# Performance work log

Measured on AMD Instinct MI355X. Metric: run time of the kernel, lower is better.

## Reference

```python
import jax, jax.numpy as jnp
import numpy as np

E, N, F = 50000, 25000, 32

def setup_inputs() -> dict:
    key = jax.random.key(0)
    ks = jax.random.split(key, 8)
    efeat = jax.random.normal(ks[0], (E, F), dtype=jnp.float32) * 0.2
    initial_efeats = jax.random.normal(ks[1], (E, F), dtype=jnp.float32) * 0.2
    # msg_fn / attn_fn: Linear(F, F*F)
    Wm = jax.random.normal(ks[2], (F * F, F), dtype=jnp.float32) * 0.05
    bm = jnp.zeros((F * F,), dtype=jnp.float32)
    Wa = jax.random.normal(ks[3], (F * F, F), dtype=jnp.float32) * 0.05
    ba = jnp.zeros((F * F,), dtype=jnp.float32)
    src = jax.random.randint(ks[4], (E,), 0, N, dtype=jnp.int32)
    dst = jax.random.randint(ks[5], (E,), 0, N, dtype=jnp.int32)
    return {"efeat": efeat, "initial_efeats": initial_efeats, "Wm": Wm, "bm": bm,
            "Wa": Wa, "ba": ba, "src": src, "dst": dst, "num_nodes": N}

def reference(efeat, initial_efeats, Wm, bm, Wa, ba, src, dst, num_nodes):
    e, f = efeat.shape
    # edge-conditioned transform matrices: [E, F, F]
    w_m = (efeat @ Wm.T + bm).reshape(e, f, f)
    w_a = (efeat @ Wa.T + ba).reshape(e, f, f)
    h = efeat[:, :, None]                 # [E, F, 1]
    ih = initial_efeats[:, :, None]       # [E, F, 1]
    e1 = w_m * h                          # [E, F, F]
    exp_e2 = jnp.exp(w_a * h)             # [E, F, F]
    initial_e1 = w_m * ih
    exp_initial_e2 = jnp.exp(w_a * ih)
    # scatter-sum exp weights to destination nodes, gather back at src
    sum_exp_node = jax.ops.segment_sum(exp_e2, dst, num_segments=num_nodes)  # [N, F, F]
    sum_exp = sum_exp_node[src] - exp_e2 + exp_initial_e2
    h1 = exp_e2 * e1
    initial_h1 = exp_initial_e2 * initial_e1
    m_node = jax.ops.segment_sum(h1, dst, num_segments=num_nodes)            # [N, F, F]
    h2 = (m_node[src] - h1 + initial_h1) / sum_exp
    return h2.sum(axis=1)                 # [E, F]
```

## Files before the change

kernel.cpp:

```cpp
#include <hip/hip_runtime.h>
#include <hip/hip_fp16.h>
#include <math.h>
#include <stdint.h>


#define FDIM   32
#define NNODES 25000

typedef __attribute__((ext_vector_type(8))) short bf16x8;
typedef __attribute__((ext_vector_type(4))) float f32x4;

__device__ __forceinline__ unsigned short f2bf(float f) {
    unsigned u = __float_as_uint(f);
    return (unsigned short)((u + 0x7FFFu + ((u >> 16) & 1u)) >> 16);
}
__device__ __forceinline__ float hlo(unsigned v) {
    return __half2float(__ushort_as_half((unsigned short)v));
}
__device__ __forceinline__ unsigned pk2(float m, float a) {
    unsigned um = (unsigned)__half_as_ushort(__float2half(m));
    unsigned ua = (unsigned)__half_as_ushort(__float2half(a));
    return (um >> 8) | (ua & 0xFF00u);
}

__global__ __launch_bounds__(256) void zero_f4(float4* __restrict__ p, int n4) {
    int i = blockIdx.x * blockDim.x + threadIdx.x;
    int stride = gridDim.x * blockDim.x;
    float4 z = make_float4(0.f, 0.f, 0.f, 0.f);
    for (; i < n4; i += stride) p[i] = z;
}

__global__ __launch_bounds__(256) void k_hist(
    const int* __restrict__ src, const int* __restrict__ dst,
    int* __restrict__ cnt_src, int* __restrict__ cnt_dst, int E) {
    int e = blockIdx.x * blockDim.x + threadIdx.x;
    if (e < E) {
        atomicAdd(&cnt_dst[dst[e]], 1);
        atomicAdd(&cnt_src[src[e]], 1);
    }
}

__global__ __launch_bounds__(256) void k_scan2(
    const int* __restrict__ cnt_dst, int* __restrict__ off_dst, int* __restrict__ cur_dst,
    const int* __restrict__ cnt_src, int* __restrict__ off_src, int* __restrict__ cur_src,
    int n) {
    const int* cnt = blockIdx.x ? cnt_src : cnt_dst;
    int* off = blockIdx.x ? off_src : off_dst;
    int* cur = blockIdx.x ? cur_src : cur_dst;
    __shared__ int wsum[4];
    __shared__ int carry_sh;
    const int tid = threadIdx.x, lane = tid & 63, w = tid >> 6;
    if (tid == 0) carry_sh = 0;
    __syncthreads();
    for (int base = 0; base < n; base += 4096) {
        int i0 = base + tid * 16;
        int v[16];
        int s = 0;
#pragma unroll
        for (int k = 0; k < 16; ++k) {
            v[k] = (i0 + k < n) ? cnt[i0 + k] : 0;
            s += v[k];
        }
        int inc = s;
        for (int d = 1; d < 64; d <<= 1) {
            int t = __shfl_up(inc, d, 64);
            if (lane >= d) inc += t;
        }
        if (lane == 63) wsum[w] = inc;
        __syncthreads();
        int wbase = 0;
        for (int k = 0; k < w; ++k) wbase += wsum[k];
        int carry = carry_sh;
        int excl = carry + wbase + inc - s;
#pragma unroll
        for (int k = 0; k < 16; ++k) {
            if (i0 + k < n) { off[i0 + k] = excl; cur[i0 + k] = excl; }
            excl += v[k];
        }
        __syncthreads();
        if (tid == 255) carry_sh = carry + wbase + inc;
    }
    __syncthreads();
    if (tid == 0) off[n] = carry_sh;
}

__global__ __launch_bounds__(256) void k_scatter(
    const int* __restrict__ src, const int* __restrict__ dst,
    int* __restrict__ cur_src, int* __restrict__ cur_dst,
    int* __restrict__ eb_src, int* __restrict__ eb_dst, int E) {
    int e = blockIdx.x * blockDim.x + threadIdx.x;
    if (e < E) {
        int p = atomicAdd(&cur_dst[dst[e]], 1); eb_dst[p] = e;
        int q = atomicAdd(&cur_src[src[e]], 1); eb_src[q] = e;
    }
}

__global__ __launch_bounds__(256) void prep_w(
    const float* __restrict__ Wm, const float* __restrict__ Wa,
    short* __restrict__ wbuf) {
    int idx = blockIdx.x * blockDim.x + threadIdx.x;
    if (idx >= 2 * 64 * 64) return;
    int mat  = idx >> 12;
    int jt   = (idx >> 6) & 63;
    int lane = idx & 63;
    const float* W = mat ? Wa : Wm;
    const float* s = W + (size_t)(jt * 16 + (lane & 15)) * FDIM + (lane >> 4) * 8;
    bf16x8 v;
#pragma unroll
    for (int t = 0; t < 8; ++t) v[t] = (short)f2bf(s[t]);
    *(bf16x8*)(wbuf + (size_t)idx * 8) = v;
}

__global__ __launch_bounds__(256) void gemm(
    const float* __restrict__ efeat,
    const float* __restrict__ bm, const float* __restrict__ ba,
    const short* __restrict__ wbuf,
    unsigned* __restrict__ buf, int E)
{
    const int lane = threadIdx.x & 63;
    const int wid  = threadIdx.x >> 6;
    const int et   = blockIdx.x * 4 + wid;
    if (et * 16 >= E) return;
    const int r16 = lane & 15;
    const int kq  = lane >> 4;

    const float* xa = efeat + (size_t)(et * 16 + r16) * FDIM + kq * 8;
    bf16x8 xfrag;
#pragma unroll
    for (int t = 0; t < 8; ++t) xfrag[t] = (short)f2bf(xa[t]);

    const int e = et * 16 + r16;
    unsigned* bout = buf + ((size_t)e << 9);

    for (int m = 0; m < 16; ++m) {
        unsigned P[4][4];
#pragma unroll
        for (int p = 0; p < 4; ++p) {
            const int jt = m * 4 + p;
            bf16x8 wfm = *(const bf16x8*)(wbuf + ((size_t)(jt)      * 64 + lane) * 8);
            bf16x8 wfa = *(const bf16x8*)(wbuf + ((size_t)(64 + jt) * 64 + lane) * 8);
            const int jb = jt * 16 + kq * 4;
            const float4 bm4 = *(const float4*)(bm + jb);
            const float4 ba4 = *(const float4*)(ba + jb);
            f32x4 accm = {bm4.x, bm4.y, bm4.z, bm4.w};
            f32x4 acca = {ba4.x, ba4.y, ba4.z, ba4.w};
            accm = __builtin_amdgcn_mfma_f32_16x16x32_bf16(wfm, xfrag, accm, 0, 0, 0);
            acca = __builtin_amdgcn_mfma_f32_16x16x32_bf16(wfa, xfrag, acca, 0, 0, 0);
#pragma unroll
            for (int r = 0; r < 4; ++r) P[p][r] = pk2(accm[r], acca[r]);
        }
        uint4 sa, sb;
        sa.x = P[0][0] | (P[2][0] << 16);
        sa.y = P[0][1] | (P[2][1] << 16);
        sa.z = P[0][2] | (P[2][2] << 16);
        sa.w = P[0][3] | (P[2][3] << 16);
        sb.x = P[1][0] | (P[3][0] << 16);
        sb.y = P[1][1] | (P[3][1] << 16);
        sb.z = P[1][2] | (P[3][2] << 16);
        sb.w = P[1][3] | (P[3][3] << 16);
        *(uint4*)(bout + m * 32 + kq * 4)      = sa;
        *(uint4*)(bout + m * 32 + 16 + kq * 4) = sb;
    }
}

__global__ __launch_bounds__(256) void consume(
    const float* __restrict__ efeat, const float* __restrict__ ifeat,
    const unsigned* __restrict__ buf,
    const int* __restrict__ off_dst, const int* __restrict__ eb_dst,
    const int* __restrict__ off_src, const int* __restrict__ eb_src,
    float* __restrict__ out)
{
    const int tid = threadIdx.x;
    const int l   = tid & 63;
    const int wid = tid >> 6;
    const int n   = blockIdx.x * 4 + wid;
    if (n >= NNODES) return;

    const int a0 = off_dst[n], a1 = off_dst[n + 1];
    const int b0 = off_src[n], b1 = off_src[n + 1];
    const int din = a1 - a0, dout = b1 - b0;
    if (dout == 0) return;

    int eid = (l < 32) ? eb_dst[a0 + l] : eb_src[b0 + (l - 32)];
    const int half = l & 1;
    const int j2   = l >> 1;
    const int mb   = half * 8;

    float S[16], M[16];
#pragma unroll
    for (int t = 0; t < 16; ++t) { S[t] = 0.f; M[t] = 0.f; }

    for (int t = 0; t < din; ++t) {
        int e = (t < 32) ? __shfl(eid, t, 64) : eb_dst[a0 + t];
        e = __builtin_amdgcn_readfirstlane(e);
        const unsigned* bp = buf + ((size_t)e << 9) + j2;
        const float* xr = efeat + ((size_t)e << 5) + half * 16;
        float xf[16];
        {
            float4 q0 = *(const float4*)(xr + 0);
            float4 q1 = *(const float4*)(xr + 4);
            float4 q2 = *(const float4*)(xr + 8);
            float4 q3 = *(const float4*)(xr + 12);
            xf[0]=q0.x; xf[1]=q0.y; xf[2]=q0.z; xf[3]=q0.w;
            xf[4]=q1.x; xf[5]=q1.y; xf[6]=q1.z; xf[7]=q1.w;
            xf[8]=q2.x; xf[9]=q2.y; xf[10]=q2.z; xf[11]=q2.w;
            xf[12]=q3.x; xf[13]=q3.y; xf[14]=q3.z; xf[15]=q3.w;
        }
#pragma unroll
        for (int s = 0; s < 8; ++s) {
            unsigned d = bp[(mb + s) * 32];
            float am0 = hlo(d << 8),  aa0 = hlo(d);
            float am1 = hlo(d >> 8),  aa1 = hlo(d >> 16);
            float xi0 = xf[2 * s], xi1 = xf[2 * s + 1];
            float ea = __expf(aa0 * xi0);
            float eb = __expf(aa1 * xi1);
            S[2 * s]     += ea;  M[2 * s]     = fmaf(ea, am0 * xi0, M[2 * s]);
            S[2 * s + 1] += eb;  M[2 * s + 1] = fmaf(eb, am1 * xi1, M[2 * s + 1]);
        }
    }

    for (int t = 0; t < dout; ++t) {
        int e = (t < 32) ? __shfl(eid, 32 + t, 64) : eb_src[b0 + t];
        e = __builtin_amdgcn_readfirstlane(e);
        const unsigned* bp = buf + ((size_t)e << 9) + j2;
        const float* xr  = efeat + ((size_t)e << 5) + half * 16;
        const float* x0r = ifeat + ((size_t)e << 5) + half * 16;
        float xf[16], x0f[16];
        {
            float4 q0 = *(const float4*)(xr + 0);
            float4 q1 = *(const float4*)(xr + 4);
            float4 q2 = *(const float4*)(xr + 8);
            float4 q3 = *(const float4*)(xr + 12);
            xf[0]=q0.x; xf[1]=q0.y; xf[2]=q0.z; xf[3]=q0.w;
            xf[4]=q1.x; xf[5]=q1.y; xf[6]=q1.z; xf[7]=q1.w;
            xf[8]=q2.x; xf[9]=q2.y; xf[10]=q2.z; xf[11]=q2.w;
            xf[12]=q3.x; xf[13]=q3.y; xf[14]=q3.z; xf[15]=q3.w;
            float4 p0 = *(const float4*)(x0r + 0);
            float4 p1 = *(const float4*)(x0r + 4);
            float4 p2 = *(const float4*)(x0r + 8);
            float4 p3 = *(const float4*)(x0r + 12);
            x0f[0]=p0.x; x0f[1]=p0.y; x0f[2]=p0.z; x0f[3]=p0.w;
            x0f[4]=p1.x; x0f[5]=p1.y; x0f[6]=p1.z; x0f[7]=p1.w;
            x0f[8]=p2.x; x0f[9]=p2.y; x0f[10]=p2.z; x0f[11]=p2.w;
            x0f[12]=p3.x; x0f[13]=p3.y; x0f[14]=p3.z; x0f[15]=p3.w;
        }
        float osum = 0.f;
#pragma unroll
        for (int s = 0; s < 8; ++s) {
            unsigned d = bp[(mb + s) * 32];
            float am0 = hlo(d << 8),  aa0 = hlo(d);
            float am1 = hlo(d >> 8),  aa1 = hlo(d >> 16);
#define PROC(T, AM, AA)                                                 \
            {                                                           \
                float xi   = xf[T];                                     \
                float x0i  = x0f[T];                                    \
                float e2   = __expf((AA) * xi);                         \
                float h1   = e2 * ((AM) * xi);                          \
                float ei2  = __expf((AA) * x0i);                        \
                float ih1  = ei2 * ((AM) * x0i);                        \
                float den  = (S[T] - e2) + ei2;                         \
                float num  = (M[T] - h1) + ih1;                         \
                float h2   = num * __builtin_amdgcn_rcpf(den);          \
                osum += isfinite(h2) ? h2 : 0.f;                        \
            }
            PROC(2 * s,     am0, aa0);
            PROC(2 * s + 1, am1, aa1);
#undef PROC
        }
        osum += __shfl_xor(osum, 1, 64);
        if (half == 0) out[((size_t)e << 5) + j2] = osum;
    }
}

extern "C" void kernel_launch(void* const* d_in, const int* in_sizes, int n_in,
                              void* d_out, int out_size, void* d_ws, size_t ws_size,
                              hipStream_t stream) {
    const float* efeat = (const float*)d_in[0];
    const float* ifeat = (const float*)d_in[1];
    const float* Wm    = (const float*)d_in[2];
    const float* bm    = (const float*)d_in[3];
    const float* Wa    = (const float*)d_in[4];
    const float* ba    = (const float*)d_in[5];
    const int*   src   = (const int*)d_in[6];
    const int*   dst   = (const int*)d_in[7];
    const int E = in_sizes[6];
    const int N = NNODES;
    float* out = (float*)d_out;

    int* cnt_dst = (int*)d_ws;
    int* cnt_src = cnt_dst + N;
    int* off_dst = cnt_src + N;
    int* off_src = off_dst + (N + 1);
    int* cur_dst = off_src + (N + 1);
    int* cur_src = cur_dst + N;
    int* eb_dst  = cur_src + N;
    int* eb_src  = eb_dst + E;
    short* wbuf  = (short*)(((uintptr_t)(eb_src + E) + 255) & ~(uintptr_t)255);
    unsigned* buf =
        (unsigned*)(((uintptr_t)(wbuf + 2 * 64 * 64 * 8) + 255) & ~(uintptr_t)255);

    zero_f4<<<64, 256, 0, stream>>>((float4*)cnt_dst, (2 * N) / 4);
    k_hist<<<(E + 255) / 256, 256, 0, stream>>>(src, dst, cnt_src, cnt_dst, E);
    k_scan2<<<2, 256, 0, stream>>>(cnt_dst, off_dst, cur_dst,
                                   cnt_src, off_src, cur_src, N);
    k_scatter<<<(E + 255) / 256, 256, 0, stream>>>(src, dst, cur_src, cur_dst,
                                                   eb_src, eb_dst, E);
    prep_w<<<32, 256, 0, stream>>>(Wm, Wa, wbuf);

    const int etiles = (E + 15) / 16;
    gemm<<<(etiles + 3) / 4, 256, 0, stream>>>(efeat, bm, ba, wbuf, buf, E);
    consume<<<(NNODES + 3) / 4, 256, 0, stream>>>(efeat, ifeat, buf,
                                                  off_dst, eb_dst,
                                                  off_src, eb_src, out);
}
```

Measured before the change: 244.2 us.

## Prescale GEMM outputs by edge features and software-pipeline consume loads

The GEMM epilogue now stores w_a*x*log2(e) and w_m*x in place of the raw weights, plus a per-edge fp16 ratio x0/x. This lets consume drop its efeat/ifeat loads and use exp2 directly. The consume loops are double-buffered so the next edge's packed data is loaded while the current one is processed. The risk is precision loss from storing prescaled values in the 8-bit packed format and from the ratio, which becomes huge or infinite when x is near zero.

```diff
diff --git a/kernel.cpp b/kernel.cpp
--- a/kernel.cpp
+++ b/kernel.cpp
@@ -17,11 +17,16 @@
 __device__ __forceinline__ float hlo(unsigned v) {
     return __half2float(__ushort_as_half((unsigned short)v));
 }
-__device__ __forceinline__ unsigned pk2(float m, float a) {
-    unsigned um = (unsigned)__half_as_ushort(__float2half(m));
-    unsigned ua = (unsigned)__half_as_ushort(__float2half(a));
-    return (um >> 8) | (ua & 0xFF00u);
-}
+__device__ __forceinline__ unsigned pk2(float q, float p) {
+    unsigned uq = (unsigned)__half_as_ushort(__float2half(q));
+    unsigned up = (unsigned)__half_as_ushort(__float2half(p));
+    return (uq >> 8) | (up & 0xFF00u);
+}
+#if __has_builtin(__builtin_amdgcn_exp2f)
+__device__ __forceinline__ float ex2(float x) { return __builtin_amdgcn_exp2f(x); }
+#else
+__device__ __forceinline__ float ex2(float x) { return exp2f(x); }
+#endif
 
 __global__ __launch_bounds__(256) void zero_f4(float4* __restrict__ p, int n4) {
     int i = blockIdx.x * blockDim.x + threadIdx.x;
@@ -112,10 +117,10 @@
 }
 
 __global__ __launch_bounds__(256) void gemm(
-    const float* __restrict__ efeat,
+    const float* __restrict__ efeat, const float* __restrict__ ifeat,
     const float* __restrict__ bm, const float* __restrict__ ba,
     const short* __restrict__ wbuf,
-    unsigned* __restrict__ buf, int E)
+    unsigned* __restrict__ buf, unsigned* __restrict__ ratio, int E)
 {
     const int lane = threadIdx.x & 63;
     const int wid  = threadIdx.x >> 6;
@@ -123,16 +128,20 @@
     if (et * 16 >= E) return;
     const int r16 = lane & 15;
     const int kq  = lane >> 4;
-
-    const float* xa = efeat + (size_t)(et * 16 + r16) * FDIM + kq * 8;
+    const int e   = et * 16 + r16;
+
+    const float* xrow  = efeat + ((size_t)e << 5);
+    const float* x0row = ifeat + ((size_t)e << 5);
+
+    const float* xa = xrow + kq * 8;
     bf16x8 xfrag;
 #pragma unroll
     for (int t = 0; t < 8; ++t) xfrag[t] = (short)f2bf(xa[t]);
 
-    const int e = et * 16 + r16;
     unsigned* bout = buf + ((size_t)e << 9);
 
     for (int m = 0; m < 16; ++m) {
+        float2 xe = *(const float2*)(xrow + 2 * m);
         unsigned P[4][4];
 #pragma unroll
         for (int p = 0; p < 4; ++p) {
@@ -146,8 +155,11 @@
             f32x4 acca = {ba4.x, ba4.y, ba4.z, ba4.w};
             accm = __builtin_amdgcn_mfma_f32_16x16x32_bf16(wfm, xfrag, accm, 0, 0, 0);
             acca = __builtin_amdgcn_mfma_f32_16x16x32_bf16(wfa, xfrag, acca, 0, 0, 0);
-#pragma unroll
-            for (int r = 0; r < 4; ++r) P[p][r] = pk2(accm[r], acca[r]);
+            const float xi  = (p >> 1) ? xe.y : xe.x;
+            const float xil = xi * 1.44269504f;
+#pragma unroll
+            for (int r = 0; r < 4; ++r)
+                P[p][r] = pk2(acca[r] * xil, accm[r] * xi);
         }
         uint4 sa, sb;
         sa.x = P[0][0] | (P[2][0] << 16);
@@ -160,12 +172,20 @@
         sb.w = P[1][3] | (P[3][3] << 16);
         *(uint4*)(bout + m * 32 + kq * 4)      = sa;
         *(uint4*)(bout + m * 32 + 16 + kq * 4) = sb;
+
+        if (kq == 0) {
+            float2 x0e = *(const float2*)(x0row + 2 * m);
+            float r0 = x0e.x * __builtin_amdgcn_rcpf(xe.x);
+            float r1 = x0e.y * __builtin_amdgcn_rcpf(xe.y);
+            unsigned h0 = (unsigned)__half_as_ushort(__float2half(r0));
+            unsigned h1 = (unsigned)__half_as_ushort(__float2half(r1));
+            ratio[((size_t)e << 4) + m] = h0 | (h1 << 16);
+        }
     }
 }
 
 __global__ __launch_bounds__(256) void consume(
-    const float* __restrict__ efeat, const float* __restrict__ ifeat,
-    const unsigned* __restrict__ buf,
+    const unsigned* __restrict__ buf, const unsigned* __restrict__ ratio,
     const int* __restrict__ off_dst, const int* __restrict__ eb_dst,
     const int* __restrict__ off_src, const int* __restrict__ eb_src,
     float* __restrict__ out)
@@ -190,86 +210,76 @@
 #pragma unroll
     for (int t = 0; t < 16; ++t) { S[t] = 0.f; M[t] = 0.f; }
 
-    for (int t = 0; t < din; ++t) {
-        int e = (t < 32) ? __shfl(eid, t, 64) : eb_dst[a0 + t];
-        e = __builtin_amdgcn_readfirstlane(e);
-        const unsigned* bp = buf + ((size_t)e << 9) + j2;
-        const float* xr = efeat + ((size_t)e << 5) + half * 16;
-        float xf[16];
-        {
-            float4 q0 = *(const float4*)(xr + 0);
-            float4 q1 = *(const float4*)(xr + 4);
-            float4 q2 = *(const float4*)(xr + 8);
-            float4 q3 = *(const float4*)(xr + 12);
-            xf[0]=q0.x; xf[1]=q0.y; xf[2]=q0.z; xf[3]=q0.w;
-            xf[4]=q1.x; xf[5]=q1.y; xf[6]=q1.z; xf[7]=q1.w;
-            xf[8]=q2.x; xf[9]=q2.y; xf[10]=q2.z; xf[11]=q2.w;
-            xf[12]=q3.x; xf[13]=q3.y; xf[14]=q3.z; xf[15]=q3.w;
-        }
-#pragma unroll
-        for (int s = 0; s < 8; ++s) {
-            unsigned d = bp[(mb + s) * 32];
-            float am0 = hlo(d << 8),  aa0 = hlo(d);
-            float am1 = hlo(d >> 8),  aa1 = hlo(d >> 16);
-            float xi0 = xf[2 * s], xi1 = xf[2 * s + 1];
-            float ea = __expf(aa0 * xi0);
-            float eb = __expf(aa1 * xi1);
-            S[2 * s]     += ea;  M[2 * s]     = fmaf(ea, am0 * xi0, M[2 * s]);
-            S[2 * s + 1] += eb;  M[2 * s + 1] = fmaf(eb, am1 * xi1, M[2 * s + 1]);
-        }
-    }
-
-    for (int t = 0; t < dout; ++t) {
-        int e = (t < 32) ? __shfl(eid, 32 + t, 64) : eb_src[b0 + t];
-        e = __builtin_amdgcn_readfirstlane(e);
-        const unsigned* bp = buf + ((size_t)e << 9) + j2;
-        const float* xr  = efeat + ((size_t)e << 5) + half * 16;
-        const float* x0r = ifeat + ((size_t)e << 5) + half * 16;
-        float xf[16], x0f[16];
-        {
-            float4 q0 = *(const float4*)(xr + 0);
-            float4 q1 = *(const float4*)(xr + 4);
-            float4 q2 = *(const float4*)(xr + 8);
-            float4 q3 = *(const float4*)(xr + 12);
-            xf[0]=q0.x; xf[1]=q0.y; xf[2]=q0.z; xf[3]=q0.w;
-            xf[4]=q1.x; xf[5]=q1.y; xf[6]=q1.z; xf[7]=q1.w;
-            xf[8]=q2.x; xf[9]=q2.y; xf[10]=q2.z; xf[11]=q2.w;
-            xf[12]=q3.x; xf[13]=q3.y; xf[14]=q3.z; xf[15]=q3.w;
-            float4 p0 = *(const float4*)(x0r + 0);
-            float4 p1 = *(const float4*)(x0r + 4);
-            float4 p2 = *(const float4*)(x0r + 8);
-            float4 p3 = *(const float4*)(x0r + 12);
-            x0f[0]=p0.x; x0f[1]=p0.y; x0f[2]=p0.z; x0f[3]=p0.w;
-            x0f[4]=p1.x; x0f[5]=p1.y; x0f[6]=p1.z; x0f[7]=p1.w;
-            x0f[8]=p2.x; x0f[9]=p2.y; x0f[10]=p2.z; x0f[11]=p2.w;
-            x0f[12]=p3.x; x0f[13]=p3.y; x0f[14]=p3.z; x0f[15]=p3.w;
-        }
-        float osum = 0.f;
-#pragma unroll
-        for (int s = 0; s < 8; ++s) {
-            unsigned d = bp[(mb + s) * 32];
-            float am0 = hlo(d << 8),  aa0 = hlo(d);
-            float am1 = hlo(d >> 8),  aa1 = hlo(d >> 16);
-#define PROC(T, AM, AA)                                                 \
-            {                                                           \
-                float xi   = xf[T];                                     \
-                float x0i  = x0f[T];                                    \
-                float e2   = __expf((AA) * xi);                         \
-                float h1   = e2 * ((AM) * xi);                          \
-                float ei2  = __expf((AA) * x0i);                        \
-                float ih1  = ei2 * ((AM) * x0i);                        \
-                float den  = (S[T] - e2) + ei2;                         \
-                float num  = (M[T] - h1) + ih1;                         \
-                float h2   = num * __builtin_amdgcn_rcpf(den);          \
-                osum += isfinite(h2) ? h2 : 0.f;                        \
-            }
-            PROC(2 * s,     am0, aa0);
-            PROC(2 * s + 1, am1, aa1);
-#undef PROC
-        }
-        osum += __shfl_xor(osum, 1, 64);
-        if (half == 0) out[((size_t)e << 5) + j2] = osum;
-    }
+#define BCIN(t)  __builtin_amdgcn_readfirstlane(((t) < 32) ? __shfl(eid, (t), 64) : eb_dst[a0 + (t)])
+#define BCOUT(t) __builtin_amdgcn_readfirstlane(((t) < 32) ? __shfl(eid, 32 + (t), 64) : eb_src[b0 + (t)])
+#define LDA(R, ee) { const unsigned* bp_ = buf + ((size_t)(ee) << 9) + j2;      \
+    _Pragma("unroll") for (int s_ = 0; s_ < 8; ++s_) R[s_] = bp_[(mb + s_) * 32]; }
+#define LDR(RF, ee) { const uint4* rp_ = (const uint4*)(ratio + (((size_t)(ee)) << 4) + mb); \
+    uint4 ra_ = rp_[0], rb_ = rp_[1];                                           \
+    RF[0] = ra_.x; RF[1] = ra_.y; RF[2] = ra_.z; RF[3] = ra_.w;                 \
+    RF[4] = rb_.x; RF[5] = rb_.y; RF[6] = rb_.z; RF[7] = rb_.w; }
+#define CIN(R) { _Pragma("unroll") for (int s_ = 0; s_ < 8; ++s_) {             \
+    unsigned d_ = R[s_];                                                        \
+    float q0_ = hlo(d_ << 8),  p0_ = hlo(d_);                                   \
+    float q1_ = hlo(d_ >> 8),  p1_ = hlo(d_ >> 16);                             \
+    float ea_ = ex2(q0_), eb_ = ex2(q1_);                                       \
+    S[2*s_]   += ea_;  M[2*s_]   = fmaf(ea_, p0_, M[2*s_]);                     \
+    S[2*s_+1] += eb_;  M[2*s_+1] = fmaf(eb_, p1_, M[2*s_+1]); } }
+#define PRC(T, Q, P, RI) {                                                      \
+    float e2_  = ex2(Q);        float h1_  = e2_ * (P);                         \
+    float ei2_ = ex2((Q)*(RI)); float ih1_ = ei2_ * ((P) * (RI));               \
+    float den_ = (S[T] - e2_) + ei2_;                                           \
+    float num_ = (M[T] - h1_) + ih1_;                                           \
+    float h2_  = num_ * __builtin_amdgcn_rcpf(den_);                            \
+    osum += isfinite(h2_) ? h2_ : 0.f; }
+#define COUT(R, RF, eo) { float osum = 0.f;                                     \
+    _Pragma("unroll") for (int s_ = 0; s_ < 8; ++s_) {                          \
+        unsigned d_ = R[s_], rw_ = RF[s_];                                      \
+        float ri0_ = hlo(rw_), ri1_ = hlo(rw_ >> 16);                           \
+        float q0_ = hlo(d_ << 8),  p0_ = hlo(d_);                               \
+        float q1_ = hlo(d_ >> 8),  p1_ = hlo(d_ >> 16);                         \
+        PRC(2*s_,     q0_, p0_, ri0_);                                          \
+        PRC(2*s_ + 1, q1_, p1_, ri1_); }                                        \
+    osum += __shfl_xor(osum, 1, 64);                                            \
+    if (half == 0) out[((size_t)(eo) << 5) + j2] = osum; }
+
+    unsigned A0[8], A1[8], R0[8], R1[8];
+
+    if (din > 0) { int e_ = BCIN(0); LDA(A0, e_); }
+    if (din > 1) { int e_ = BCIN(1); LDA(A1, e_); }
+    {
+        int t = 0;
+        while (t < din) {
+            CIN(A0);
+            if (t + 2 < din) { int e_ = BCIN(t + 2); LDA(A0, e_); }
+            if (t + 1 >= din) break;
+            CIN(A1);
+            if (t + 3 < din) { int e_ = BCIN(t + 3); LDA(A1, e_); }
+            t += 2;
+        }
+    }
+
+    int eo0 = 0, eo1 = 0;
+    if (dout > 0) { eo0 = BCOUT(0); LDA(A0, eo0); LDR(R0, eo0); }
+    if (dout > 1) { eo1 = BCOUT(1); LDA(A1, eo1); LDR(R1, eo1); }
+    {
+        int t = 0;
+        while (t < dout) {
+            COUT(A0, R0, eo0);
+            if (t + 2 < dout) { eo0 = BCOUT(t + 2); LDA(A0, eo0); LDR(R0, eo0); }
+            if (t + 1 >= dout) break;
+            COUT(A1, R1, eo1);
+            if (t + 3 < dout) { eo1 = BCOUT(t + 3); LDA(A1, eo1); LDR(R1, eo1); }
+            t += 2;
+        }
+    }
+#undef BCIN
+#undef BCOUT
+#undef LDA
+#undef LDR
+#undef CIN
+#undef PRC
+#undef COUT
 }
 
 extern "C" void kernel_launch(void* const* d_in, const int* in_sizes, int n_in,
@@ -298,6 +308,7 @@
     short* wbuf  = (short*)(((uintptr_t)(eb_src + E) + 255) & ~(uintptr_t)255);
     unsigned* buf =
         (unsigned*)(((uintptr_t)(wbuf + 2 * 64 * 64 * 8) + 255) & ~(uintptr_t)255);
+    unsigned* ratio = buf + (size_t)E * 512;
 
     zero_f4<<<64, 256, 0, stream>>>((float4*)cnt_dst, (2 * N) / 4);
     k_hist<<<(E + 255) / 256, 256, 0, stream>>>(src, dst, cnt_src, cnt_dst, E);
@@ -308,8 +319,9 @@
     prep_w<<<32, 256, 0, stream>>>(Wm, Wa, wbuf);
 
     const int etiles = (E + 15) / 16;
-    gemm<<<(etiles + 3) / 4, 256, 0, stream>>>(efeat, bm, ba, wbuf, buf, E);
-    consume<<<(NNODES + 3) / 4, 256, 0, stream>>>(efeat, ifeat, buf,
+    gemm<<<(etiles + 3) / 4, 256, 0, stream>>>(efeat, ifeat, bm, ba, wbuf,
+                                               buf, ratio, E);
+    consume<<<(NNODES + 3) / 4, 256, 0, stream>>>(buf, ratio,
                                                   off_dst, eb_dst,
                                                   off_src, eb_src, out);
 }
```

After: 238.1 us. 1.03x faster.
